# Optimization experiments

Measured on AMD Instinct MI355X. Metric: run time of the kernel, lower is better.

## Reference

```python
import jax, jax.numpy as jnp
import numpy as np

LEAKY_SLOPE = 0.2
NEG_INF = -9e15
LN_EPS = 1e-5


def conv1x1(x, W, b):
    # x: [B, Cin, N, L], W: [Cout, Cin], b: [Cout] -> [B, Cout, N, L]
    return jnp.einsum('bcnl,oc->bonl', x, W) + b[None, :, None, None]


def gat_layer(h, mask, W, a, concat):
    # h: [B, L, N, Fin], mask: [N, N] bool, W: [Fin, Fout], a: [2*Fout, 1]
    Wh = h @ W                                   # [B, L, N, Fout]
    F_out = W.shape[1]
    Wh1 = Wh @ a[:F_out]                         # [B, L, N, 1]
    Wh2 = Wh @ a[F_out:]                         # [B, L, N, 1]
    e = jax.nn.leaky_relu(Wh1 + jnp.swapaxes(Wh2, -1, -2), LEAKY_SLOPE)  # [B,L,N,N]
    att = jnp.where(mask, e, NEG_INF)
    att = jax.nn.softmax(att, axis=-1)
    h_prime = att @ Wh                           # [B, L, N, Fout]
    return jax.nn.elu(h_prime) if concat else h_prime


def custom_layernorm(x):
    # normalizes over dims (1, 2) as in the torch LayerNorm (affine disabled)
    m = x.mean(axis=(1, 2), keepdims=True)
    v = x.var(axis=(1, 2), keepdims=True)
    return (x - m) / jnp.sqrt(v + LN_EPS)


def setup_inputs() -> dict:
    key = jax.random.key(0)
    ks = jax.random.split(key, 16)
    B, C, N, L = 4, 256, 1024, 12
    s = 0.06  # ~xavier scale for 256-dim fans
    return {
        'x_in': jax.random.normal(ks[0], (B, C, N, L), dtype=jnp.float32),
        'D_Graph': jax.random.randint(ks[1], (N, N), 0, 2, dtype=jnp.int32),
        'nodevec1': jax.random.normal(ks[2], (N, 6), dtype=jnp.float32),
        'nodevec2': jax.random.normal(ks[3], (6, N), dtype=jnp.float32),
        'W_mlp': jax.random.normal(ks[4], (C, 2 * C), dtype=jnp.float32) * 0.04,
        'b_mlp': jnp.zeros((C,), dtype=jnp.float32),
        'W_g0': jax.random.normal(ks[5], (C, C), dtype=jnp.float32) * s,
        'a_g0': jax.random.normal(ks[6], (2 * C, 1), dtype=jnp.float32) * s,
        'W_go': jax.random.normal(ks[7], (C, C), dtype=jnp.float32) * s,
        'a_go': jax.random.normal(ks[8], (2 * C, 1), dtype=jnp.float32) * s,
        'Wg1': jax.random.normal(ks[9], (C, C), dtype=jnp.float32) * s,
        'bg1': jnp.zeros((C,), dtype=jnp.float32),
        'Wg2': jax.random.normal(ks[10], (C, C), dtype=jnp.float32) * s,
        'bg2': jnp.zeros((C,), dtype=jnp.float32),
        'Wg3': jax.random.normal(ks[11], (C, C), dtype=jnp.float32) * s,
        'bg3': jnp.zeros((C,), dtype=jnp.float32),
        'alpha': jnp.float32(-5.0),
        'weight': jnp.ones((C, N, 1), dtype=jnp.float32),
        'bias': jnp.zeros((C, N, 1), dtype=jnp.float32),
    }


def reference(x_in, D_Graph, nodevec1, nodevec2, W_mlp, b_mlp, W_g0, a_g0,
              W_go, a_go, Wg1, bg1, Wg2, bg2, Wg3, bg3, alpha, weight, bias):
    # --- adaptive-adjacency GCN branch (support_len=1, order=1) ---
    adp = jax.nn.softmax(jax.nn.relu(nodevec1 @ nodevec2), axis=1)  # [N, N]
    x1 = jnp.einsum('bcvl,wv->bcwl', x_in, adp)
    h = jnp.concatenate([x_in, x1], axis=1)                         # [B, 2C, N, L]
    x_gcn = conv1x1(h, W_mlp, b_mlp)                                # [B, C, N, L]

    # --- dense adjacency-masked GAT branch (nheads=1, order=1) ---
    mask = D_Graph > 0
    ht = jnp.transpose(x_in, (0, 3, 2, 1))                          # [B, L, N, C]
    g = gat_layer(ht, mask, W_g0, a_g0, concat=True)
    g = jax.nn.elu(gat_layer(g, mask, W_go, a_go, concat=False))
    x_gat = jnp.transpose(g, (0, 3, 2, 1))                          # [B, C, N, L]

    # --- fuse, residual, norm, GLU, affine ---
    a_s = jax.nn.sigmoid(alpha)
    x = a_s * x_gat + (1.0 - a_s) * x_gcn + x_in
    x = custom_layernorm(x)
    g1 = conv1x1(x, Wg1, bg1)
    g2 = conv1x1(x, Wg2, bg2)
    glu_out = conv1x1(g1 * jax.nn.sigmoid(g2), Wg3, bg3)
    x = glu_out + x
    x = x * weight[None] + bias[None] + x
    x = custom_layernorm(x)
    return x
```

## Files before the change

### kernel.cpp

```cpp
#include <hip/hip_runtime.h>
#include <hip/hip_bf16.h>
#include <math.h>

#define DI __device__ __forceinline__
#define AS1 __attribute__((address_space(1)))
#define AS3 __attribute__((address_space(3)))

static constexpr int  B_ = 4, C_ = 256, N_ = 1024, L_ = 12, BL_ = 48;
static constexpr long SLAB = (long)N_ * C_;
static constexpr long TOT  = (long)BL_ * SLAB;

typedef __attribute__((ext_vector_type(8))) short bf16x8;
typedef __attribute__((ext_vector_type(4))) float f32x4;

DI float b2f(uint hw) { return __builtin_bit_cast(float, (hw & 0xffffu) << 16); }
DI ushort f2b(float f) {
    uint u = __builtin_bit_cast(uint, f);
    u += 0x7FFFu + ((u >> 16) & 1u);
    return (ushort)(u >> 16);
}
DI uint pack2(float a, float b) {
    __hip_bfloat162 h = __float22bfloat162_rn(make_float2(a, b));
    uint r;
    __builtin_memcpy(&r, &h, 4);
    return r;
}

DI void gload16(const void* g, void* l) {
    __builtin_amdgcn_global_load_lds((AS1 uint*)g, (AS3 uint*)l, 16, 0, 0);
}

DI float block_sum256(float v, float* sc) {
    #pragma unroll
    for (int o = 32; o > 0; o >>= 1) v += __shfl_xor(v, o, 64);
    int wid = threadIdx.x >> 6;
    __syncthreads();
    if ((threadIdx.x & 63) == 0) sc[wid] = v;
    __syncthreads();
    return sc[0] + sc[1] + sc[2] + sc[3];
}
DI float block_max256(float v, float* sc) {
    #pragma unroll
    for (int o = 32; o > 0; o >>= 1) v = fmaxf(v, __shfl_xor(v, o, 64));
    int wid = threadIdx.x >> 6;
    __syncthreads();
    if ((threadIdx.x & 63) == 0) sc[wid] = v;
    __syncthreads();
    return fmaxf(fmaxf(sc[0], sc[1]), fmaxf(sc[2], sc[3]));
}

__global__ __launch_bounds__(256) void k_adp(const float* __restrict__ nv1,
                                             const float* __restrict__ nv2,
                                             ushort* __restrict__ adp) {
    __shared__ float r[6];
    __shared__ float sc[4];
    int row = blockIdx.x, tid = threadIdx.x;
    if (tid < 6) r[tid] = nv1[row * 6 + tid];
    __syncthreads();
    float e[4];
    #pragma unroll
    for (int q = 0; q < 4; q++) {
        int j = tid + q * 256;
        float s = 0.f;
        #pragma unroll
        for (int k = 0; k < 6; k++) s += r[k] * nv2[k * 1024 + j];
        e[q] = s > 0.f ? s : 0.f;
    }
    float m = fmaxf(fmaxf(e[0], e[1]), fmaxf(e[2], e[3]));
    m = block_max256(m, sc);
    float ps = 0.f;
    #pragma unroll
    for (int q = 0; q < 4; q++) { e[q] = __expf(e[q] - m); ps += e[q]; }
    ps = block_sum256(ps, sc);
    float rinv = 1.f / ps;
    #pragma unroll
    for (int q = 0; q < 4; q++) adp[(long)row * 1024 + tid + q * 256] = f2b(e[q] * rinv);
}

__global__ __launch_bounds__(256) void k_tin(const float* __restrict__ x,
                                             ushort* __restrict__ xb,
                                             float* __restrict__ xf) {
    __shared__ float t[64][65];
    int nl0 = blockIdx.x * 64, c0 = blockIdx.y * 64, b = blockIdx.z;
    int lx = threadIdx.x & 63, ly = threadIdx.x >> 6;
    #pragma unroll
    for (int i = 0; i < 16; i++) {
        int c = c0 + ly + i * 4;
        t[ly + i * 4][lx] = x[(long)(b * 256 + c) * 12288 + nl0 + lx];
    }
    __syncthreads();
    #pragma unroll
    for (int i = 0; i < 16; i++) {
        int nl = nl0 + ly + i * 4;
        int n = nl / 12, l = nl % 12;
        long idx = ((long)(b * 12 + l) * 1024 + n) * 256 + c0 + lx;
        float v = t[lx][ly + i * 4];
        xb[idx] = f2b(v);
        xf[idx] = v;
    }
}

__global__ __launch_bounds__(256) void k_xtt(const ushort* __restrict__ X,
                                             ushort* __restrict__ XT) {
    __shared__ ushort t[64][68];
    int bl = blockIdx.z;
    int n0 = blockIdx.x * 64, c0 = blockIdx.y * 64;
    int lx = threadIdx.x & 63, ly = threadIdx.x >> 6;
    const ushort* Xp = X + (long)bl * SLAB;
    #pragma unroll
    for (int i = 0; i < 16; i++)
        t[ly + i * 4][lx] = Xp[(long)(n0 + ly + i * 4) * 256 + c0 + lx];
    __syncthreads();
    ushort* Tp = XT + (long)bl * SLAB;
    #pragma unroll
    for (int i = 0; i < 16; i++)
        Tp[(long)(c0 + ly + i * 4) * 1024 + n0 + lx] = t[lx][ly + i * 4];
}

__global__ __launch_bounds__(256) void k_wt2(const float* __restrict__ S0, ushort* __restrict__ D0,
                                             const float* __restrict__ S1, ushort* __restrict__ D1) {
    __shared__ float t[64][65];
    const float* S = blockIdx.z ? S1 : S0;
    ushort* D = blockIdx.z ? D1 : D0;
    int c0 = blockIdx.x * 64, o0 = blockIdx.y * 64;
    int lx = threadIdx.x & 63, ly = threadIdx.x >> 6;
    #pragma unroll
    for (int i = 0; i < 16; i++)
        t[ly + i * 4][lx] = S[(long)(c0 + ly + i * 4) * 256 + o0 + lx];
    __syncthreads();
    #pragma unroll
    for (int i = 0; i < 16; i++)
        D[(long)(o0 + ly + i * 4) * 256 + c0 + lx] = f2b(t[lx][ly + i * 4]);
}

__global__ __launch_bounds__(256) void k_wconv(const float* __restrict__ S, ushort* __restrict__ D) {
    long i = (long)blockIdx.x * 256 + threadIdx.x;
    D[i] = f2b(S[i]);
}

__global__ __launch_bounds__(256) void k_wgi(const float* __restrict__ W1, const float* __restrict__ b1,
                                             const float* __restrict__ W2, const float* __restrict__ b2,
                                             ushort* __restrict__ WGI, float* __restrict__ BI) {
    int n = blockIdx.x, p = n >> 5, q = n & 31;
    const float* src = (q < 16) ? W1 + (long)(p * 16 + q) * 256
                                : W2 + (long)(p * 16 + q - 16) * 256;
    WGI[(long)n * 256 + threadIdx.x] = f2b(src[threadIdx.x]);
    if (threadIdx.x == 0) BI[n] = (q < 16) ? b1[p * 16 + q] : b2[p * 16 + q - 16];
}

__global__ __launch_bounds__(256) void k_va(const float* __restrict__ W, const float* __restrict__ a,
                                            float* __restrict__ va) {
    __shared__ float sc[4];
    int c = blockIdx.x, t = threadIdx.x;
    float w = W[(long)c * 256 + t];
    float s1 = block_sum256(w * a[t], sc);
    float s2 = block_sum256(w * a[256 + t], sc);
    if (t == 0) { va[c] = s1; va[256 + c] = s2; }
}

__global__ __launch_bounds__(256) void k_wtprep(const float* __restrict__ w,
                                                const float* __restrict__ b,
                                                float* __restrict__ wt,
                                                float* __restrict__ bt) {
    int n = blockIdx.x, c = threadIdx.x;
    wt[(long)n * 256 + c] = w[(long)c * 1024 + n] + 1.f;
    bt[(long)n * 256 + c] = b[(long)c * 1024 + n];
}

__global__ __launch_bounds__(256) void k_maskpack(const int* __restrict__ dg,
                                                  uint* __restrict__ maskw) {
    int w = blockIdx.x * 256 + threadIdx.x;
    int row = w >> 5, wo = w & 31;
    uint m = 0;
    #pragma unroll
    for (int b = 0; b < 32; b++)
        m |= (dg[(long)row * 1024 + wo * 32 + b] > 0 ? 1u : 0u) << b;
    maskw[w] = m;
}

template<int NPAIR, int GLU>
__global__ __launch_bounds__(256) void k_bgemm(
    const ushort* __restrict__ A0, long sA0,
    const ushort* __restrict__ A1, long sA1,
    int lda, int K0, int KK,
    const ushort* __restrict__ Bt, long sBt,
    const float* __restrict__ bias,
    float* __restrict__ Cf, ushort* __restrict__ Cb, long sC,
    const float* __restrict__ biasi) {
    __shared__ ushort As[128 * 32];
    __shared__ ushort Bs[128 * 32];
    const int tid = threadIdx.x;
    const int bl = blockIdx.z;
    const int m0 = blockIdx.x * 128, n0 = blockIdx.y * 128;
    const int N = gridDim.y * 128;
    const int lane = tid & 63, w = tid >> 6;
    const int wm = (w >> 1) * 64, wn = (w & 1) * 64;
    const int sr = tid >> 2, sk = (tid & 3) * 8;
    const int fr = lane & 15, fk = (lane >> 4) * 8;
    f32x4 acc[4][4] = {};
    const ushort* Ab0 = A0 + (long)bl * sA0;
    const ushort* Ab1 = (NPAIR == 2) ? A1 + (long)bl * sA1 : nullptr;
    const ushort* Bb = Bt + (long)bl * sBt;
    for (int k0 = 0; k0 < KK; k0 += 32) {
        const ushort* Asrc = Ab0; int kl = k0;
        if (NPAIR == 2 && k0 >= K0) { Asrc = Ab1; kl = k0 - K0; }
        __syncthreads();
        gload16(&Asrc[(long)(m0 + sr) * lda + kl + sk],      &As[sr * 32 + sk]);
        gload16(&Asrc[(long)(m0 + sr + 64) * lda + kl + sk], &As[(sr + 64) * 32 + sk]);
        gload16(&Bb[(long)(n0 + sr) * KK + k0 + sk],         &Bs[sr * 32 + sk]);
        gload16(&Bb[(long)(n0 + sr + 64) * KK + k0 + sk],    &Bs[(sr + 64) * 32 + sk]);
        __syncthreads();
        bf16x8 af[4], bg[4];
        #pragma unroll
        for (int i = 0; i < 4; i++) {
            af[i] = *(const bf16x8*)&As[(wm + i * 16 + fr) * 32 + fk];
            bg[i] = *(const bf16x8*)&Bs[(wn + i * 16 + fr) * 32 + fk];
        }
        #pragma unroll
        for (int i = 0; i < 4; i++)
            #pragma unroll
            for (int j = 0; j < 4; j++)
                acc[i][j] = __builtin_amdgcn_mfma_f32_16x16x32_bf16(af[i], bg[j], acc[i][j], 0, 0, 0);
    }
    const int cn = lane & 15, rb = (lane >> 4) * 4;
    if (GLU) {
        #pragma unroll
        for (int nt = 0; nt < 4; nt += 2) {
            int n1 = n0 + wn + nt * 16 + cn;
            int hcol = ((n1 >> 5) << 4) + cn;
            float b1 = biasi[n1], b2 = biasi[n1 + 16];
            #pragma unroll
            for (int i = 0; i < 4; i++) {
                #pragma unroll
                for (int r = 0; r < 4; r++) {
                    int m = m0 + wm + i * 16 + rb + r;
                    float g1 = acc[i][nt][r] + b1;
                    float g2 = acc[i][nt + 1][r] + b2;
                    float h = g1 / (1.f + __expf(-g2));
                    Cb[(long)bl * sC + (long)m * 256 + hcol] = f2b(h);
                }
            }
        }
    } else {
        #pragma unroll
        for (int j = 0; j < 4; j++) {
            int n = n0 + wn + j * 16 + cn;
            float bv = bias ? bias[n] : 0.f;
            #pragma unroll
            for (int i = 0; i < 4; i++) {
                #pragma unroll
                for (int r = 0; r < 4; r++) {
                    int m = m0 + wm + i * 16 + rb + r;
                    float v = acc[i][j][r] + bv;
                    long idx = (long)bl * sC + (long)m * N + n;
                    if (Cf) Cf[idx] = v;
                    if (Cb) Cb[idx] = f2b(v);
                }
            }
        }
    }
}

__global__ __launch_bounds__(256) void k_dots(const ushort* __restrict__ X,
                                              const float* __restrict__ va,
                                              float* __restrict__ o1,
                                              float* __restrict__ o2) {
    int wid = threadIdx.x >> 6, lane = threadIdx.x & 63;
    long row = (long)blockIdx.x * 4 + wid;
    uint2 xv = *(const uint2*)(X + row * 256 + lane * 4);
    float x0 = b2f(xv.x), x1 = b2f(xv.x >> 16), x2 = b2f(xv.y), x3 = b2f(xv.y >> 16);
    float4 v1 = *(const float4*)&va[lane * 4];
    float4 v2 = *(const float4*)&va[256 + lane * 4];
    float s1 = x0 * v1.x + x1 * v1.y + x2 * v1.z + x3 * v1.w;
    float s2 = x0 * v2.x + x1 * v2.y + x2 * v2.z + x3 * v2.w;
    #pragma unroll
    for (int o = 32; o > 0; o >>= 1) { s1 += __shfl_xor(s1, o, 64); s2 += __shfl_xor(s2, o, 64); }
    if (lane == 0) { o1[row] = s1; o2[row] = s2; }
}

__global__ __launch_bounds__(256) void k_w2max(const float* __restrict__ w2v,
                                               float* __restrict__ w2m) {
    __shared__ float sc[4];
    int bl = blockIdx.x;
    float4 v = *(const float4*)&w2v[(long)bl * 1024 + threadIdx.x * 4];
    float m = fmaxf(fmaxf(v.x, v.y), fmaxf(v.z, v.w));
    m = block_max256(m, sc);
    if (threadIdx.x == 0) w2m[bl] = m;
}

__global__ __launch_bounds__(256) void k_attn_mf(
    const ushort* __restrict__ WhT,
    const float* __restrict__ w1v, const float* __restrict__ w2v,
    const float* __restrict__ w2m,
    const uint* __restrict__ maskw,
    ushort* __restrict__ outB) {
    __shared__ ushort P2[32 * 64 * 8];
    __shared__ float w2s[1024];
    __shared__ float w1s[64];
    __shared__ uint msk[64 * 33];
    __shared__ float psum[4][64];
    __shared__ float rsv[64];
    int d = blockIdx.x;
    int lidx = (d & 7) * 96 + (d >> 3);
    int bl = lidx >> 4;
    int i0 = (lidx & 15) * 64;
    int tid = threadIdx.x;
    #pragma unroll
    for (int q = 0; q < 4; q++) w2s[tid + q * 256] = w2v[(long)bl * 1024 + tid + q * 256];
    if (tid < 64) w1s[tid] = w1v[(long)bl * 1024 + i0 + tid];
    {
        const uint4* gm = (const uint4*)(maskw + (long)i0 * 32);
        uint4 ma = gm[tid * 2], mb = gm[tid * 2 + 1];
        int r0 = tid >> 2, w0 = (tid & 3) * 8;
        uint* mp = &msk[r0 * 33 + w0];
        mp[0] = ma.x; mp[1] = ma.y; mp[2] = ma.z; mp[3] = ma.w;
        mp[4] = mb.x; mp[5] = mb.y; mp[6] = mb.z; mp[7] = mb.w;
    }
    __syncthreads();
    const int row = tid & 63, jt = tid >> 6;
    const float w1r = w1s[row];
    float e0 = w1r + w2m[bl];
    const float mr = (e0 > 0.f) ? e0 : 0.2f * e0;
    float sloc = 0.f;
    const int lane = tid & 63, w = tid >> 6;
    const int wn = w * 64;
    const int fr = lane & 15, fk8 = (lane >> 4) * 8;
    f32x4 acc[4][4] = {};
    const ushort* bp = WhT + (long)bl * SLAB;
    #pragma unroll 1
    for (int jc = 0; jc < 4; jc++) {
        int j0 = jc * 256;
        uint mw0 = msk[row * 33 + jc * 8 + jt * 2];
        uint mw1 = msk[row * 33 + jc * 8 + jt * 2 + 1];
        #pragma unroll
        for (int u = 0; u < 8; u++) {
            uint mg = ((u & 4) ? mw1 : mw0) >> ((u & 3) * 8);
            int jb = j0 + jt * 64 + u * 8;
            float p[8];
            #pragma unroll
            for (int t = 0; t < 8; t++) {
                float e = w1r + w2s[jb + t];
                e = (e > 0.f) ? e : 0.2f * e;
                float pp = __expf(e - mr);
                p[t] = ((mg >> t) & 1) ? pp : 0.f;
                sloc += p[t];
            }
            uint4 pv;
            pv.x = pack2(p[0], p[1]);
            pv.y = pack2(p[2], p[3]);
            pv.z = pack2(p[4], p[5]);
            pv.w = pack2(p[6], p[7]);
            *(uint4*)((char*)P2 + ((jt * 8 + u) * 64 + row) * 16) = pv;
        }
        __syncthreads();
        #pragma unroll
        for (int ks = 0; ks < 8; ks++) {
            int kb = ks * 32 + fk8;
            bf16x8 bg[4], af[4];
            #pragma unroll
            for (int nt = 0; nt < 4; nt++)
                bg[nt] = *(const bf16x8*)&bp[(long)(wn + nt * 16 + fr) * 1024 + j0 + kb];
            int kq = ks * 4 + (lane >> 4);
            #pragma unroll
            for (int mt = 0; mt < 4; mt++)
                af[mt] = *(const bf16x8*)((char*)P2 + (kq * 64 + mt * 16 + fr) * 16);
            #pragma unroll
            for (int mt = 0; mt < 4; mt++)
                #pragma unroll
                for (int nt = 0; nt < 4; nt++)
                    acc[mt][nt] = __builtin_amdgcn_mfma_f32_16x16x32_bf16(
                        af[mt], bg[nt], acc[mt][nt], 0, 0, 0);
        }
        __syncthreads();
    }
    psum[jt][row] = sloc;
    __syncthreads();
    if (tid < 64)
        rsv[tid] = 1.f / (psum[0][tid] + psum[1][tid] + psum[2][tid] + psum[3][tid]);
    __syncthreads();
    #pragma unroll
    for (int mt = 0; mt < 4; mt++) {
        #pragma unroll
        for (int r = 0; r < 4; r++) {
            int i = mt * 16 + (lane >> 4) * 4 + r;
            float sc = rsv[i];
            #pragma unroll
            for (int nt = 0; nt < 4; nt++) {
                int c = wn + nt * 16 + fr;
                float v = acc[mt][nt][r] * sc;
                v = (v > 0.f) ? v : __expf(v) - 1.f;
                outB[(long)bl * SLAB + (long)(i0 + i) * 256 + c] = f2b(v);
            }
        }
    }
}

__global__ __launch_bounds__(256) void k_fuse_ln(const ushort* __restrict__ gat,
                                                 const float4* __restrict__ gcn,
                                                 const float4* __restrict__ xf,
                                                 const float* __restrict__ alpha,
                                                 float4* __restrict__ o,
                                                 float2* __restrict__ part) {
    __shared__ float sc[4];
    int bl = blockIdx.y;
    long i = (long)bl * 65536 + blockIdx.x * 256 + threadIdx.x;
    float as = 1.f / (1.f + __expf(-alpha[0]));
    float bs = 1.f - as;
    uint2 hv = ((const uint2*)gat)[i];
    float4 g = gcn[i], x = xf[i];
    float4 v = make_float4(as * b2f(hv.x) + bs * g.x + x.x,
                           as * b2f(hv.x >> 16) + bs * g.y + x.y,
                           as * b2f(hv.y) + bs * g.z + x.z,
                           as * b2f(hv.y >> 16) + bs * g.w + x.w);
    o[i] = v;
    float s = v.x + v.y + v.z + v.w;
    float q = v.x * v.x + v.y * v.y + v.z * v.z + v.w * v.w;
    s = block_sum256(s, sc);
    q = block_sum256(q, sc);
    if (threadIdx.x == 0) part[bl * 256 + blockIdx.x] = make_float2(s, q);
}

__global__ __launch_bounds__(256) void k_stats256(const float2* __restrict__ part,
                                                  float2* __restrict__ stats) {
    __shared__ float sc[4];
    int bl = blockIdx.x;
    float2 v = part[bl * 256 + threadIdx.x];
    float s = block_sum256(v.x, sc);
    float q = block_sum256(v.y, sc);
    if (threadIdx.x == 0) {
        float mean = s / (float)SLAB;
        float var = q / (float)SLAB - mean * mean;
        stats[bl] = make_float2(mean, 1.f / sqrtf(var + 1e-5f));
    }
}

__global__ __launch_bounds__(256) void k_ln_apply(const float4* __restrict__ x,
                                                  const float2* __restrict__ stats,
                                                  float4* __restrict__ o,
                                                  ushort* __restrict__ ob) {
    long i = (long)blockIdx.x * 256 + threadIdx.x;
    int bl = (int)(i >> 16);
    float2 st = stats[bl];
    float4 v = x[i];
    float o0 = (v.x - st.x) * st.y, o1 = (v.y - st.x) * st.y;
    float o2 = (v.z - st.x) * st.y, o3 = (v.w - st.x) * st.y;
    o[i] = make_float4(o0, o1, o2, o3);
    uint2 ow;
    ow.x = pack2(o0, o1);
    ow.y = pack2(o2, o3);
    ((uint2*)ob)[i] = ow;
}

__global__ __launch_bounds__(256) void k_finpre_ln(const float4* __restrict__ glu,
                                                   const float4* __restrict__ xn,
                                                   const float4* __restrict__ wt,
                                                   const float4* __restrict__ bt,
                                                   float4* __restrict__ o,
                                                   float2* __restrict__ part) {
    __shared__ float sc[4];
    int bl = blockIdx.y;
    long i = (long)bl * 65536 + blockIdx.x * 256 + threadIdx.x;
    long wi = i & 65535;
    float4 g = glu[i], x = xn[i], w = wt[wi], b = bt[wi];
    float4 v = make_float4((g.x + x.x) * w.x + b.x, (g.y + x.y) * w.y + b.y,
                           (g.z + x.z) * w.z + b.z, (g.w + x.w) * w.w + b.w);
    o[i] = v;
    float s = v.x + v.y + v.z + v.w;
    float q = v.x * v.x + v.y * v.y + v.z * v.z + v.w * v.w;
    s = block_sum256(s, sc);
    q = block_sum256(q, sc);
    if (threadIdx.x == 0) part[bl * 256 + blockIdx.x] = make_float2(s, q);
}

__global__ __launch_bounds__(256) void k_out(const float* __restrict__ x,
                                             const float2* __restrict__ stats,
                                             float* __restrict__ out) {
    int n = blockIdx.x, b = blockIdx.y, c = threadIdx.x;
    float v[12];
    #pragma unroll
    for (int l = 0; l < 12; l++) {
        float2 st = stats[b * 12 + l];
        float t = x[(long)(b * 12 + l) * SLAB + (long)n * 256 + c];
        v[l] = (t - st.x) * st.y;
    }
    float4* op = (float4*)(out + ((long)(b * 256 + c) * 1024 + n) * 12);
    op[0] = make_float4(v[0], v[1], v[2], v[3]);
    op[1] = make_float4(v[4], v[5], v[6], v[7]);
    op[2] = make_float4(v[8], v[9], v[10], v[11]);
}

extern "C" void kernel_launch(void* const* d_in, const int* in_sizes, int n_in,
                              void* d_out, int out_size, void* d_ws, size_t ws_size,
                              hipStream_t stream) {
    (void)in_sizes; (void)n_in; (void)out_size; (void)ws_size;
    const float* x_in = (const float*)d_in[0];
    const int*   dg   = (const int*)d_in[1];
    const float* nv1  = (const float*)d_in[2];
    const float* nv2  = (const float*)d_in[3];
    const float* Wmlp = (const float*)d_in[4];
    const float* bmlp = (const float*)d_in[5];
    const float* Wg0  = (const float*)d_in[6];
    const float* ag0  = (const float*)d_in[7];
    const float* Wgo  = (const float*)d_in[8];
    const float* ago  = (const float*)d_in[9];
    const float* Wg1  = (const float*)d_in[10];
    const float* bg1  = (const float*)d_in[11];
    const float* Wg2  = (const float*)d_in[12];
    const float* bg2  = (const float*)d_in[13];
    const float* Wg3  = (const float*)d_in[14];
    const float* bg3  = (const float*)d_in[15];
    const float* alpha = (const float*)d_in[16];
    const float* wgt  = (const float*)d_in[17];
    const float* bia  = (const float*)d_in[18];
    float* out = (float*)d_out;

    float* XTf = (float*)d_ws;
    float* Bf  = XTf + TOT;
    ushort* U1 = (ushort*)(Bf + TOT);
    ushort* U2 = U1 + TOT;
    float* Af  = (float*)U1;
    ushort* U3 = U2 + TOT;
    ushort* U4 = U3 + TOT;
    ushort* ADPB = U4 + TOT;
    ushort* WMLPB = ADPB + (long)1024 * 1024;
    ushort* WG0T = WMLPB + 131072;
    ushort* WGOT = WG0T + 65536;
    ushort* WGIB = WGOT + 65536;
    ushort* WG3B = WGIB + 131072;
    float* BIASI = (float*)(WG3B + 65536);
    float* VA = BIASI + 512;
    float* W1V = VA + 1024;
    float* W2V = W1V + 49152;
    float* W2M = W2V + 49152;
    uint* MASKW = (uint*)(W2M + 64);
    float2* PART = (float2*)(MASKW + 32768);
    float2* STATS = PART + 48 * 256;
    float* WT = (float*)(STATS + 48);
    float* BT2 = WT + SLAB;

    dim3 blk(256);
    k_wt2<<<dim3(4, 4, 2), blk, 0, stream>>>(Wg0, WG0T, Wgo, WGOT);
    k_wconv<<<512, blk, 0, stream>>>(Wmlp, WMLPB);
    k_wconv<<<256, blk, 0, stream>>>(Wg3, WG3B);
    k_wgi<<<512, blk, 0, stream>>>(Wg1, bg1, Wg2, bg2, WGIB, BIASI);
    k_va<<<256, blk, 0, stream>>>(Wg0, ag0, VA);
    k_va<<<256, blk, 0, stream>>>(Wgo, ago, VA + 512);
    k_wtprep<<<1024, blk, 0, stream>>>(wgt, bia, WT, BT2);
    k_adp<<<1024, blk, 0, stream>>>(nv1, nv2, ADPB);
    k_maskpack<<<128, blk, 0, stream>>>(dg, MASKW);
    k_tin<<<dim3(192, 4, 4), blk, 0, stream>>>(x_in, U1, XTf);
    k_xtt<<<dim3(16, 4, 48), blk, 0, stream>>>(U1, U2);
    k_bgemm<1, 0><<<dim3(8, 2, 48), blk, 0, stream>>>(ADPB, 0, nullptr, 0, 1024, 0, 1024,
                                                      U2, SLAB, nullptr, nullptr, U3, SLAB, nullptr);
    k_bgemm<2, 0><<<dim3(8, 2, 48), blk, 0, stream>>>(U1, SLAB, U3, SLAB, 256, 256, 512,
                                                      WMLPB, 0, bmlp, Bf, nullptr, SLAB, nullptr);
    k_dots<<<12288, blk, 0, stream>>>(U1, VA, W1V, W2V);
    k_w2max<<<48, blk, 0, stream>>>(W2V, W2M);
    k_bgemm<1, 0><<<dim3(2, 8, 48), blk, 0, stream>>>(WG0T, 0, nullptr, 0, 256, 0, 256,
                                                      U1, SLAB, nullptr, nullptr, U4, SLAB, nullptr);
    k_attn_mf<<<768, blk, 0, stream>>>(U4, W1V, W2V, W2M, MASKW, U2);
    k_dots<<<12288, blk, 0, stream>>>(U2, VA + 512, W1V, W2V);
    k_w2max<<<48, blk, 0, stream>>>(W2V, W2M);
    k_bgemm<1, 0><<<dim3(2, 8, 48), blk, 0, stream>>>(WGOT, 0, nullptr, 0, 256, 0, 256,
                                                      U2, SLAB, nullptr, nullptr, U4, SLAB, nullptr);
    k_attn_mf<<<768, blk, 0, stream>>>(U4, W1V, W2V, W2M, MASKW, U3);
    k_fuse_ln<<<dim3(256, 48), blk, 0, stream>>>(U3, (const float4*)Bf, (const float4*)XTf,
                                                 alpha, (float4*)Af, PART);
    k_stats256<<<48, blk, 0, stream>>>(PART, STATS);
    k_ln_apply<<<12288, blk, 0, stream>>>((const float4*)Af, STATS, (float4*)Bf, U3);
    k_bgemm<1, 1><<<dim3(8, 4, 48), blk, 0, stream>>>(U3, SLAB, nullptr, 0, 256, 0, 256,
                                                      WGIB, 0, nullptr, nullptr, U4, SLAB, BIASI);
    k_bgemm<1, 0><<<dim3(8, 2, 48), blk, 0, stream>>>(U4, SLAB, nullptr, 0, 256, 0, 256,
                                                      WG3B, 0, bg3, XTf, nullptr, SLAB, nullptr);
    k_finpre_ln<<<dim3(256, 48), blk, 0, stream>>>((const float4*)XTf, (const float4*)Bf,
                                                   (const float4*)WT, (const float4*)BT2,
                                                   (float4*)Af, PART);
    k_stats256<<<48, blk, 0, stream>>>(PART, STATS);
    k_out<<<dim3(1024, 4), blk, 0, stream>>>(Af, STATS, out);
}
```

Measured before the change: 511.4 us.

## Double-buffer GEMM LDS tiles, shrink attention chunk, drop fp32 LN output write

The batched bf16 GEMM now double-buffers its LDS A/B tiles, so the next K-slice load is issued before computing the current one and one barrier per iteration is removed. The attention kernel processes 128-column chunks instead of 256, halving its P buffer in LDS and asking for 4 blocks per CU to raise occupancy. The first layernorm no longer writes a full fp32 normalized tensor; the later residual kernel recomputes normalization from the pre-norm buffer and stats. The trade-offs are doubled GEMM LDS, more attention barriers, and an extra stats read.

Result: no change. 502.2 us (-1.8%).

```diff
diff --git a/kernel.cpp b/kernel.cpp
--- a/kernel.cpp
+++ b/kernel.cpp
@@ -187,8 +187,8 @@
     const float* __restrict__ bias,
     float* __restrict__ Cf, ushort* __restrict__ Cb, long sC,
     const float* __restrict__ biasi) {
-    __shared__ ushort As[128 * 32];
-    __shared__ ushort Bs[128 * 32];
+    __shared__ ushort As[2][128 * 32];
+    __shared__ ushort Bs[2][128 * 32];
     const int tid = threadIdx.x;
     const int bl = blockIdx.z;
     const int m0 = blockIdx.x * 128, n0 = blockIdx.y * 128;
@@ -201,27 +201,40 @@
     const ushort* Ab0 = A0 + (long)bl * sA0;
     const ushort* Ab1 = (NPAIR == 2) ? A1 + (long)bl * sA1 : nullptr;
     const ushort* Bb = Bt + (long)bl * sBt;
-    for (int k0 = 0; k0 < KK; k0 += 32) {
+
+    auto stage = [&](int buf, int k0) {
         const ushort* Asrc = Ab0; int kl = k0;
         if (NPAIR == 2 && k0 >= K0) { Asrc = Ab1; kl = k0 - K0; }
-        __syncthreads();
-        gload16(&Asrc[(long)(m0 + sr) * lda + kl + sk],      &As[sr * 32 + sk]);
-        gload16(&Asrc[(long)(m0 + sr + 64) * lda + kl + sk], &As[(sr + 64) * 32 + sk]);
-        gload16(&Bb[(long)(n0 + sr) * KK + k0 + sk],         &Bs[sr * 32 + sk]);
-        gload16(&Bb[(long)(n0 + sr + 64) * KK + k0 + sk],    &Bs[(sr + 64) * 32 + sk]);
-        __syncthreads();
+        gload16(&Asrc[(long)(m0 + sr) * lda + kl + sk],      &As[buf][sr * 32 + sk]);
+        gload16(&Asrc[(long)(m0 + sr + 64) * lda + kl + sk], &As[buf][(sr + 64) * 32 + sk]);
+        gload16(&Bb[(long)(n0 + sr) * KK + k0 + sk],         &Bs[buf][sr * 32 + sk]);
+        gload16(&Bb[(long)(n0 + sr + 64) * KK + k0 + sk],    &Bs[buf][(sr + 64) * 32 + sk]);
+    };
+    auto compute = [&](int buf) {
         bf16x8 af[4], bg[4];
         #pragma unroll
         for (int i = 0; i < 4; i++) {
-            af[i] = *(const bf16x8*)&As[(wm + i * 16 + fr) * 32 + fk];
-            bg[i] = *(const bf16x8*)&Bs[(wn + i * 16 + fr) * 32 + fk];
+            af[i] = *(const bf16x8*)&As[buf][(wm + i * 16 + fr) * 32 + fk];
+            bg[i] = *(const bf16x8*)&Bs[buf][(wn + i * 16 + fr) * 32 + fk];
         }
         #pragma unroll
         for (int i = 0; i < 4; i++)
             #pragma unroll
             for (int j = 0; j < 4; j++)
                 acc[i][j] = __builtin_amdgcn_mfma_f32_16x16x32_bf16(af[i], bg[j], acc[i][j], 0, 0, 0);
-    }
+    };
+
+    stage(0, 0);
+    __syncthreads();
+    int cur = 0;
+    for (int k0 = 32; k0 < KK; k0 += 32) {
+        stage(cur ^ 1, k0);
+        compute(cur);
+        __syncthreads();
+        cur ^= 1;
+    }
+    compute(cur);
+
     const int cn = lane & 15, rb = (lane >> 4) * 4;
     if (GLU) {
         #pragma unroll
@@ -288,13 +301,13 @@
     if (threadIdx.x == 0) w2m[bl] = m;
 }
 
-__global__ __launch_bounds__(256) void k_attn_mf(
+__global__ __launch_bounds__(256, 4) void k_attn_mf(
     const ushort* __restrict__ WhT,
     const float* __restrict__ w1v, const float* __restrict__ w2v,
     const float* __restrict__ w2m,
     const uint* __restrict__ maskw,
     ushort* __restrict__ outB) {
-    __shared__ ushort P2[32 * 64 * 8];
+    __shared__ ushort P2[16 * 64 * 8];
     __shared__ float w2s[1024];
     __shared__ float w1s[64];
     __shared__ uint msk[64 * 33];
@@ -328,14 +341,13 @@
     f32x4 acc[4][4] = {};
     const ushort* bp = WhT + (long)bl * SLAB;
     #pragma unroll 1
-    for (int jc = 0; jc < 4; jc++) {
-        int j0 = jc * 256;
-        uint mw0 = msk[row * 33 + jc * 8 + jt * 2];
-        uint mw1 = msk[row * 33 + jc * 8 + jt * 2 + 1];
-        #pragma unroll
-        for (int u = 0; u < 8; u++) {
-            uint mg = ((u & 4) ? mw1 : mw0) >> ((u & 3) * 8);
-            int jb = j0 + jt * 64 + u * 8;
+    for (int jc = 0; jc < 8; jc++) {
+        int j0 = jc * 128;
+        uint mw = msk[row * 33 + jc * 4 + jt];
+        #pragma unroll
+        for (int u = 0; u < 4; u++) {
+            uint mg = mw >> (u * 8);
+            int jb = j0 + jt * 32 + u * 8;
             float p[8];
             #pragma unroll
             for (int t = 0; t < 8; t++) {
@@ -350,11 +362,11 @@
             pv.y = pack2(p[2], p[3]);
             pv.z = pack2(p[4], p[5]);
             pv.w = pack2(p[6], p[7]);
-            *(uint4*)((char*)P2 + ((jt * 8 + u) * 64 + row) * 16) = pv;
+            *(uint4*)((char*)P2 + ((jt * 4 + u) * 64 + row) * 16) = pv;
         }
         __syncthreads();
         #pragma unroll
-        for (int ks = 0; ks < 8; ks++) {
+        for (int ks = 0; ks < 4; ks++) {
             int kb = ks * 32 + fk8;
             bf16x8 bg[4], af[4];
             #pragma unroll
@@ -436,23 +448,20 @@
 
 __global__ __launch_bounds__(256) void k_ln_apply(const float4* __restrict__ x,
                                                   const float2* __restrict__ stats,
-                                                  float4* __restrict__ o,
                                                   ushort* __restrict__ ob) {
     long i = (long)blockIdx.x * 256 + threadIdx.x;
     int bl = (int)(i >> 16);
     float2 st = stats[bl];
     float4 v = x[i];
-    float o0 = (v.x - st.x) * st.y, o1 = (v.y - st.x) * st.y;
-    float o2 = (v.z - st.x) * st.y, o3 = (v.w - st.x) * st.y;
-    o[i] = make_float4(o0, o1, o2, o3);
     uint2 ow;
-    ow.x = pack2(o0, o1);
-    ow.y = pack2(o2, o3);
+    ow.x = pack2((v.x - st.x) * st.y, (v.y - st.x) * st.y);
+    ow.y = pack2((v.z - st.x) * st.y, (v.w - st.x) * st.y);
     ((uint2*)ob)[i] = ow;
 }
 
 __global__ __launch_bounds__(256) void k_finpre_ln(const float4* __restrict__ glu,
-                                                   const float4* __restrict__ xn,
+                                                   const float4* __restrict__ afull,
+                                                   const float2* __restrict__ stats1,
                                                    const float4* __restrict__ wt,
                                                    const float4* __restrict__ bt,
                                                    float4* __restrict__ o,
@@ -461,9 +470,12 @@
     int bl = blockIdx.y;
     long i = (long)bl * 65536 + blockIdx.x * 256 + threadIdx.x;
     long wi = i & 65535;
-    float4 g = glu[i], x = xn[i], w = wt[wi], b = bt[wi];
-    float4 v = make_float4((g.x + x.x) * w.x + b.x, (g.y + x.y) * w.y + b.y,
-                           (g.z + x.z) * w.z + b.z, (g.w + x.w) * w.w + b.w);
+    float2 st = stats1[bl];
+    float4 g = glu[i], a = afull[i], w = wt[wi], b = bt[wi];
+    float4 v = make_float4((g.x + (a.x - st.x) * st.y) * w.x + b.x,
+                           (g.y + (a.y - st.x) * st.y) * w.y + b.y,
+                           (g.z + (a.z - st.x) * st.y) * w.z + b.z,
+                           (g.w + (a.w - st.x) * st.y) * w.w + b.w);
     o[i] = v;
     float s = v.x + v.y + v.z + v.w;
     float q = v.x * v.x + v.y * v.y + v.z * v.z + v.w * v.w;
@@ -567,14 +579,14 @@
     k_fuse_ln<<<dim3(256, 48), blk, 0, stream>>>(U3, (const float4*)Bf, (const float4*)XTf,
                                                  alpha, (float4*)Af, PART);
     k_stats256<<<48, blk, 0, stream>>>(PART, STATS);
-    k_ln_apply<<<12288, blk, 0, stream>>>((const float4*)Af, STATS, (float4*)Bf, U3);
+    k_ln_apply<<<12288, blk, 0, stream>>>((const float4*)Af, STATS, U3);
     k_bgemm<1, 1><<<dim3(8, 4, 48), blk, 0, stream>>>(U3, SLAB, nullptr, 0, 256, 0, 256,
                                                       WGIB, 0, nullptr, nullptr, U4, SLAB, BIASI);
     k_bgemm<1, 0><<<dim3(8, 2, 48), blk, 0, stream>>>(U4, SLAB, nullptr, 0, 256, 0, 256,
                                                       WG3B, 0, bg3, XTf, nullptr, SLAB, nullptr);
-    k_finpre_ln<<<dim3(256, 48), blk, 0, stream>>>((const float4*)XTf, (const float4*)Bf,
-                                                   (const float4*)WT, (const float4*)BT2,
-                                                   (float4*)Af, PART);
+    k_finpre_ln<<<dim3(256, 48), blk, 0, stream>>>((const float4*)XTf, (const float4*)Af,
+                                                   STATS, (const float4*)WT, (const float4*)BT2,
+                                                   (float4*)Bf, PART);
     k_stats256<<<48, blk, 0, stream>>>(PART, STATS);
-    k_out<<<dim3(1024, 4), blk, 0, stream>>>(Af, STATS, out);
-}
+    k_out<<<dim3(1024, 4), blk, 0, stream>>>(Bf, STATS, out);
+}
```
